# Kernel tuning notes

Hardware: AMD Instinct MI355X
Metric: run time of the kernel (lower is better)

Reference implementation:

```python
import jax, jax.numpy as jnp
import numpy as np

H = 8  # LSTM units, from LSTM_Cell(8)
D = 32  # input feature dim
B = 256
T = 2048


def setup_inputs() -> dict:
    key = jax.random.key(0)
    k1, k2, k3 = jax.random.split(key, 3)
    x = jax.random.normal(k1, (B, T, D), dtype=jnp.float32)
    h0 = jnp.zeros((B, H), dtype=jnp.float32)
    c0 = jnp.zeros((B, H), dtype=jnp.float32)
    # standard LSTM cell params: gate order i, f, g (candidate), o
    Wx = jax.random.normal(k2, (D, 4 * H), dtype=jnp.float32) * (1.0 / np.sqrt(D))
    Wh = jax.random.normal(k3, (H, 4 * H), dtype=jnp.float32) * (1.0 / np.sqrt(H))
    b = jnp.zeros((4 * H,), dtype=jnp.float32)
    return {"x": x, "h0": h0, "c0": c0, "Wx": Wx, "Wh": Wh, "b": b}


def reference(x, h0, c0, Wx, Wh, b):
    """Unrolled LSTM recurrence over time, expressed as a fused lax.scan.

    Returns the per-timestep hidden states [B, T, H] (same math as the
    Python-loop layer, which collects h_t for every t) plus final (h, c).
    """
    xs = jnp.transpose(x, (1, 0, 2))  # [T, B, D]

    def step(carry, xt):
        h, c = carry
        z = xt @ Wx + h @ Wh + b  # [B, 4H]
        i, f, g, o = jnp.split(z, 4, axis=-1)
        i = jax.nn.sigmoid(i)
        f = jax.nn.sigmoid(f)
        g = jnp.tanh(g)
        o = jax.nn.sigmoid(o)
        c_new = f * c + i * g
        h_new = o * jnp.tanh(c_new)
        return (h_new, c_new), h_new

    (h_f, c_f), hs = jax.lax.scan(step, (h0, c0), xs)
    outputs = jnp.transpose(hs, (1, 0, 2))  # [B, T, H]
    return outputs, h_f, c_f
```

## Files before the change

kernel.cpp:

```cpp
#include <hip/hip_runtime.h>
#include <hip/hip_fp16.h>

#define T_STEPS 2048
#define BATCH   256

__device__ __forceinline__ float fexp2(float x) {
#if __has_builtin(__builtin_amdgcn_exp2f)
  return __builtin_amdgcn_exp2f(x);
#else
  return exp2f(x);
#endif
}
__device__ __forceinline__ float frcp(float x) {
#if __has_builtin(__builtin_amdgcn_rcpf)
  return __builtin_amdgcn_rcpf(x);
#else
  return 1.0f / x;
#endif
}

template<int CTRL>
__device__ __forceinline__ float dppf(float x) {
  int i = __float_as_int(x);
  int r = __builtin_amdgcn_update_dpp(i, i, CTRL, 0xF, 0xF, false);
  return __int_as_float(r);
}
#define DPP_X1 0xB1
#define DPP_X2 0x4E
#define DPP_HM 0x141
#define DPP_RM 0x140

#define PIN(x) asm volatile("" : "+v"(x))

#define L2E 1.442695040888963f

__global__ __launch_bounds__(256, 4) void zx_kernel(const float* __restrict__ x,
                                                    const float* __restrict__ Wx,
                                                    const float* __restrict__ bias,
                                                    unsigned* __restrict__ zx) {
  __shared__ float sWx[1024];
  __shared__ float sb[32];
  {
    int t = (int)threadIdx.x;
    for (int i = t; i < 1024; i += 256) sWx[i] = Wx[i];
    if (t < 32) sb[t] = bias[t];
  }
  __syncthreads();

  int wave = (blockIdx.x * 256 + (int)threadIdx.x) >> 6;
  int lane = (int)threadIdx.x & 63;
  int l    = lane & 31;
  int r    = lane >> 5;
  int j    = (l & 3) * 8 + (l >> 2);

  float wxc[32];
#pragma unroll
  for (int d = 0; d < 32; ++d) wxc[d] = sWx[d * 32 + j];
  float bj = sb[j];

  int base = wave * 64;

  for (int it = 0; it < 32; ++it) {
#pragma unroll
    for (int d = 0; d < 32; ++d) PIN(wxc[d]);
    PIN(bj);
    int row = base + (it << 1) + r;
    const float4* xr = (const float4*)(x + (size_t)row * 32);
    float a = bj, b2 = 0.0f;
#pragma unroll
    for (int qq = 0; qq < 8; ++qq) {
      float4 v = xr[qq];
      a  = fmaf(v.x, wxc[4*qq+0], a);
      b2 = fmaf(v.y, wxc[4*qq+1], b2);
      a  = fmaf(v.z, wxc[4*qq+2], a);
      b2 = fmaf(v.w, wxc[4*qq+3], b2);
    }
    float v  = a + b2;
    float pv = dppf<DPP_X1>(v);
    float lo = (l & 1) ? pv : v;
    float hi = (l & 1) ? v  : pv;
    union { _Float16 h2[2]; unsigned u; } pk;
    pk.h2[0] = (_Float16)lo;
    pk.h2[1] = (_Float16)hi;
    zx[(size_t)row * 16 + (l >> 1)] = pk.u;
  }
}

__global__ __launch_bounds__(64, 1) void lstm_kernel(const __half* __restrict__ zx,
                                                     const float* __restrict__ h0,
                                                     const float* __restrict__ c0,
                                                     const float* __restrict__ Wh,
                                                     float* __restrict__ out) {
  __shared__ float sWh[256];
  int lane = (int)threadIdx.x;
  for (int i = lane; i < 256; i += 64) sWh[i] = Wh[i];
  __syncthreads();

  int b = blockIdx.x * 4 + (lane >> 4);
  int q = lane & 15;
  int u = q >> 1;
  int p = q & 1;
  bool pb = (p != 0);

  float wA[8], wB[8];
#pragma unroll
  for (int m = 0; m < 8; ++m) {
    int jrow = u ^ m;
    wA[m] = sWh[jrow * 32 + (2 * p) * 8 + u];
    wB[m] = sWh[jrow * 32 + (2 * p + 1) * 8 + u];
  }
  float cAc = pb ? -2.0f * L2E : -L2E;
  float aAc = pb ? 2.0f : 1.0f;
  float bAc = pb ? -1.0f : 0.0f;

  float h = h0[b * 8 + u];
  float c = c0[b * 8 + u];

  const unsigned* zcur = (const unsigned*)zx + (size_t)b * T_STEPS * 16 + u * 2 + p;
  float*          ocur = out + (size_t)b * T_STEPS * 8 + u;

  constexpr int PD = 8;
  unsigned buf[PD];
#pragma unroll
  for (int pp = 0; pp < PD; ++pp) buf[pp] = zcur[pp * 16];

#define STEP(pp, PRE)                                                        \
  {                                                                          \
    union { unsigned u32; __half2 h2; } zz; zz.u32 = buf[pp];                \
    float2 zf = __half22float2(zz.h2);         \
    if (PRE) buf[pp] = zcur[(pp + PD) * 16];                                 \
    float r0 = h;                                       \
    float r1 = dppf<DPP_X2>(r0);                        \
    float r3 = dppf<DPP_HM>(r0);                        \
    float r7 = dppf<DPP_RM>(r0);                        \
    float r2 = dppf<DPP_X2>(r3);                        \
    float r6 = dppf<DPP_X2>(r7);                        \
    float r4 = dppf<DPP_HM>(r7);                        \
    float r5 = dppf<DPP_X2>(r4);                        \
    float A0 = fmaf(r0, wA[0], zf.x);    \
    float B0 = fmaf(r0, wB[0], zf.y);                                        \
    float A1 = r1 * wA[1];                                                   \
    float B1 = r1 * wB[1];                                                   \
    A1 = fmaf(r3, wA[3], A1);  B1 = fmaf(r3, wB[3], B1);                     \
    A0 = fmaf(r2, wA[2], A0);  B0 = fmaf(r2, wB[2], B0);                     \
    A1 = fmaf(r7, wA[7], A1);  B1 = fmaf(r7, wB[7], B1);                     \
    A0 = fmaf(r6, wA[6], A0);  B0 = fmaf(r6, wB[6], B0);                     \
    A0 = fmaf(r4, wA[4], A0);  B0 = fmaf(r4, wB[4], B0);                     \
    A1 = fmaf(r5, wA[5], A1);  B1 = fmaf(r5, wB[5], B1);                     \
    float A = A0 + A1, B = B0 + B1;                                          \
    float Aact = fmaf(aAc, frcp(1.0f + fexp2(cAc * A)), bAc);                \
    float Bact = frcp(1.0f + fexp2(-L2E * B));                               \
    float A2 = dppf<DPP_X1>(Aact);                                           \
    float B2 = dppf<DPP_X1>(Bact);                                           \
    float iv = pb ? A2   : Aact;                                             \
    float fv = pb ? B2   : Bact;                                             \
    float gv = pb ? Aact : A2;                                               \
    float ov = pb ? Bact : B2;                                               \
    c = fmaf(fv, c, iv * gv);                                                \
    float th = fmaf(2.0f, frcp(1.0f + fexp2(-2.0f * L2E * c)), -1.0f);       \
    h = ov * th;                                                             \
    ocur[pp * 8] = h;            \
  }

  for (int tb = 0; tb < T_STEPS - PD; tb += PD) {
#pragma unroll
    for (int m = 0; m < 8; ++m) { PIN(wA[m]); PIN(wB[m]); }
    PIN(cAc); PIN(aAc); PIN(bAc);
    STEP(0, 1) STEP(1, 1) STEP(2, 1) STEP(3, 1)
    STEP(4, 1) STEP(5, 1) STEP(6, 1) STEP(7, 1)
    zcur += PD * 16;
    ocur += PD * 8;
  }
  STEP(0, 0) STEP(1, 0) STEP(2, 0) STEP(3, 0)
  STEP(4, 0) STEP(5, 0) STEP(6, 0) STEP(7, 0)
#undef STEP

  out[(size_t)BATCH * T_STEPS * 8 +             b * 8 + u] = h;
  out[(size_t)BATCH * T_STEPS * 8 + BATCH * 8 + b * 8 + u] = c;
}

extern "C" void kernel_launch(void* const* d_in, const int* in_sizes, int n_in,
                              void* d_out, int out_size, void* d_ws, size_t ws_size,
                              hipStream_t stream) {
  const float* x    = (const float*)d_in[0];
  const float* h0   = (const float*)d_in[1];
  const float* c0   = (const float*)d_in[2];
  const float* Wx   = (const float*)d_in[3];
  const float* Wh   = (const float*)d_in[4];
  const float* bias = (const float*)d_in[5];
  float* out = (float*)d_out;

  zx_kernel<<<2048, 256, 0, stream>>>(x, Wx, bias, (unsigned*)d_ws);
  lstm_kernel<<<BATCH / 4, 64, 0, stream>>>((const __half*)d_ws, h0, c0, Wh, out);
}
```

Baseline: 421.0 us.

## Hand-schedule LSTM recurrence loop in inline GCN assembly

Replaces the compiler-generated serial LSTM step loop with a hand-written inline-assembly loop. It uses explicit DPP gathers, exp/rcp activations, cndmask gate selection on a precomputed vcc, manual s_nop hazard padding, vmcnt waits and offset-addressed global loads and stores. The aim is to shorten the per-timestep dependency chain and cut scheduling overhead on the latency-bound recurrence. It also rewrites the g gate as 2*sigmoid(2x)-1 fused into the c update and the tanh as fma(2, sig, -o) to save instructions. The risks are fragile hazard handling, hand-placed waitcnts, and 32-bit offsets that must not overflow.

```diff
diff --git a/kernel.cpp b/kernel.cpp
--- a/kernel.cpp
+++ b/kernel.cpp
@@ -3,21 +3,6 @@
 
 #define T_STEPS 2048
 #define BATCH   256
-
-__device__ __forceinline__ float fexp2(float x) {
-#if __has_builtin(__builtin_amdgcn_exp2f)
-  return __builtin_amdgcn_exp2f(x);
-#else
-  return exp2f(x);
-#endif
-}
-__device__ __forceinline__ float frcp(float x) {
-#if __has_builtin(__builtin_amdgcn_rcpf)
-  return __builtin_amdgcn_rcpf(x);
-#else
-  return 1.0f / x;
-#endif
-}
 
 template<int CTRL>
 __device__ __forceinline__ float dppf(float x) {
@@ -26,12 +11,7 @@
   return __int_as_float(r);
 }
 #define DPP_X1 0xB1
-#define DPP_X2 0x4E
-#define DPP_HM 0x141
-#define DPP_RM 0x140
-
 #define PIN(x) asm volatile("" : "+v"(x))
-
 #define L2E 1.442695040888963f
 
 __global__ __launch_bounds__(256, 4) void zx_kernel(const float* __restrict__ x,
@@ -59,7 +39,6 @@
   float bj = sb[j];
 
   int base = wave * 64;
-
   for (int it = 0; it < 32; ++it) {
 #pragma unroll
     for (int d = 0; d < 32; ++d) PIN(wxc[d]);
@@ -86,6 +65,79 @@
   }
 }
 
+
+#define GATHER_DOTS \
+  "v_mov_b32_dpp %[tC], %[h] quad_perm:[2,3,0,1] row_mask:0xf bank_mask:0xf\n\t" \
+  "v_mov_b32_dpp %[tD], %[h] row_half_mirror row_mask:0xf bank_mask:0xf\n\t" \
+  "v_mov_b32_dpp %[tE], %[h] row_mirror row_mask:0xf bank_mask:0xf\n\t" \
+  "v_fmac_f32 %[tA], %[h], %[wA0]\n\t" \
+  "v_fmac_f32 %[tB], %[h], %[wB0]\n\t" \
+  "v_mov_b32_dpp %[tF], %[tD] quad_perm:[2,3,0,1] row_mask:0xf bank_mask:0xf\n\t" \
+  "v_mul_f32 %[tG], %[tC], %[wA1]\n\t" \
+  "v_mul_f32 %[tH], %[tC], %[wB1]\n\t" \
+  "v_mov_b32_dpp %[tC], %[tE] quad_perm:[2,3,0,1] row_mask:0xf bank_mask:0xf\n\t" \
+  "v_fmac_f32 %[tG], %[tD], %[wA3]\n\t" \
+  "v_fmac_f32 %[tH], %[tD], %[wB3]\n\t" \
+  "v_mov_b32_dpp %[tD], %[tE] row_half_mirror row_mask:0xf bank_mask:0xf\n\t" \
+  "v_fmac_f32 %[tA], %[tF], %[wA2]\n\t" \
+  "v_fmac_f32 %[tB], %[tF], %[wB2]\n\t" \
+  "v_fmac_f32 %[tG], %[tE], %[wA7]\n\t" \
+  "v_fmac_f32 %[tH], %[tE], %[wB7]\n\t" \
+  "v_mov_b32_dpp %[tE], %[tD] quad_perm:[2,3,0,1] row_mask:0xf bank_mask:0xf\n\t" \
+  "v_fmac_f32 %[tA], %[tC], %[wA6]\n\t" \
+  "v_fmac_f32 %[tB], %[tC], %[wB6]\n\t" \
+  "v_fmac_f32 %[tA], %[tD], %[wA4]\n\t" \
+  "v_fmac_f32 %[tB], %[tD], %[wB4]\n\t" \
+  "v_fmac_f32 %[tG], %[tE], %[wA5]\n\t" \
+  "v_fmac_f32 %[tH], %[tE], %[wB5]\n\t"
+
+#define ACTPART \
+  "v_add_f32 %[tA], %[tA], %[tG]\n\t" \
+  "v_add_f32 %[tB], %[tB], %[tH]\n\t" \
+  "v_mul_f32 %[tC], %[cAc], %[tA]\n\t" \
+  "v_mul_f32 %[tD], 0xbfb8aa3b, %[tB]\n\t" \
+  "v_exp_f32 %[tC], %[tC]\n\t" \
+  "v_exp_f32 %[tD], %[tD]\n\t" \
+  "s_nop 0\n\t" \
+  "v_add_f32 %[tC], 1.0, %[tC]\n\t" \
+  "v_add_f32 %[tD], 1.0, %[tD]\n\t" \
+  "v_rcp_f32 %[tC], %[tC]\n\t" \
+  "v_rcp_f32 %[tD], %[tD]\n\t" \
+  "s_nop 1\n\t" \
+  "v_mov_b32_dpp %[tE], %[tD] quad_perm:[1,0,3,2] row_mask:0xf bank_mask:0xf\n\t" \
+  "v_mov_b32_dpp %[tF], %[tC] quad_perm:[1,0,3,2] row_mask:0xf bank_mask:0xf\n\t" \
+  "v_cndmask_b32 %[tG], %[tD], %[tE], vcc\n\t" \
+  "v_cndmask_b32 %[tH], %[tE], %[tD], vcc\n\t" \
+  "v_cndmask_b32 %[tE], %[tC], %[tF], vcc\n\t" \
+  "v_mul_f32 %[tF], %[tC], %[tF]\n\t" \
+  "v_fma_f32 %[tF], 2.0, %[tF], -%[tE]\n\t" \
+  "v_fma_f32 %[c], %[tG], %[c], %[tF]\n\t" \
+  "v_mul_f32 %[tA], 0xc038aa3b, %[c]\n\t" \
+  "v_exp_f32 %[tA], %[tA]\n\t" \
+  "s_nop 0\n\t" \
+  "v_add_f32 %[tA], 1.0, %[tA]\n\t" \
+  "v_rcp_f32 %[tA], %[tA]\n\t" \
+  "s_nop 0\n\t" \
+  "v_mul_f32 %[tB], %[tH], %[tA]\n\t" \
+  "v_fma_f32 %[h], 2.0, %[tB], -%[tH]\n\t"
+
+#define LSTEP(K, PF, SO) \
+  "s_waitcnt vmcnt(7)\n\t" \
+  "v_cvt_f32_f16 %[tA], %[b" #K "]\n\t" \
+  "v_lshrrev_b32 %[tB], 16, %[b" #K "]\n\t" \
+  "v_cvt_f32_f16 %[tB], %[tB]\n\t" \
+  "global_load_dword %[b" #K "], %[zoff], %[zb] offset:" #PF "\n\t" \
+  GATHER_DOTS ACTPART \
+  "global_store_dword %[ooff], %[h], %[ob] offset:" #SO "\n\t"
+
+#define ESTEP(K, SO) \
+  "s_waitcnt vmcnt(7)\n\t" \
+  "v_cvt_f32_f16 %[tA], %[b" #K "]\n\t" \
+  "v_lshrrev_b32 %[tB], 16, %[b" #K "]\n\t" \
+  "v_cvt_f32_f16 %[tB], %[tB]\n\t" \
+  GATHER_DOTS ACTPART \
+  "global_store_dword %[ooff], %[h], %[ob] offset:" #SO "\n\t"
+
 __global__ __launch_bounds__(64, 1) void lstm_kernel(const __half* __restrict__ zx,
                                                      const float* __restrict__ h0,
                                                      const float* __restrict__ c0,
@@ -100,7 +152,6 @@
   int q = lane & 15;
   int u = q >> 1;
   int p = q & 1;
-  bool pb = (p != 0);
 
   float wA[8], wB[8];
 #pragma unroll
@@ -109,71 +160,67 @@
     wA[m] = sWh[jrow * 32 + (2 * p) * 8 + u];
     wB[m] = sWh[jrow * 32 + (2 * p + 1) * 8 + u];
   }
-  float cAc = pb ? -2.0f * L2E : -L2E;
-  float aAc = pb ? 2.0f : 1.0f;
-  float bAc = pb ? -1.0f : 0.0f;
+  float cAc = p ? (-2.0f * L2E) : (-L2E);
 
   float h = h0[b * 8 + u];
   float c = c0[b * 8 + u];
 
-  const unsigned* zcur = (const unsigned*)zx + (size_t)b * T_STEPS * 16 + u * 2 + p;
-  float*          ocur = out + (size_t)b * T_STEPS * 8 + u;
-
-  constexpr int PD = 8;
-  unsigned buf[PD];
-#pragma unroll
-  for (int pp = 0; pp < PD; ++pp) buf[pp] = zcur[pp * 16];
-
-#define STEP(pp, PRE)                                                        \
-  {                                                                          \
-    union { unsigned u32; __half2 h2; } zz; zz.u32 = buf[pp];                \
-    float2 zf = __half22float2(zz.h2);         \
-    if (PRE) buf[pp] = zcur[(pp + PD) * 16];                                 \
-    float r0 = h;                                       \
-    float r1 = dppf<DPP_X2>(r0);                        \
-    float r3 = dppf<DPP_HM>(r0);                        \
-    float r7 = dppf<DPP_RM>(r0);                        \
-    float r2 = dppf<DPP_X2>(r3);                        \
-    float r6 = dppf<DPP_X2>(r7);                        \
-    float r4 = dppf<DPP_HM>(r7);                        \
-    float r5 = dppf<DPP_X2>(r4);                        \
-    float A0 = fmaf(r0, wA[0], zf.x);    \
-    float B0 = fmaf(r0, wB[0], zf.y);                                        \
-    float A1 = r1 * wA[1];                                                   \
-    float B1 = r1 * wB[1];                                                   \
-    A1 = fmaf(r3, wA[3], A1);  B1 = fmaf(r3, wB[3], B1);                     \
-    A0 = fmaf(r2, wA[2], A0);  B0 = fmaf(r2, wB[2], B0);                     \
-    A1 = fmaf(r7, wA[7], A1);  B1 = fmaf(r7, wB[7], B1);                     \
-    A0 = fmaf(r6, wA[6], A0);  B0 = fmaf(r6, wB[6], B0);                     \
-    A0 = fmaf(r4, wA[4], A0);  B0 = fmaf(r4, wB[4], B0);                     \
-    A1 = fmaf(r5, wA[5], A1);  B1 = fmaf(r5, wB[5], B1);                     \
-    float A = A0 + A1, B = B0 + B1;                                          \
-    float Aact = fmaf(aAc, frcp(1.0f + fexp2(cAc * A)), bAc);                \
-    float Bact = frcp(1.0f + fexp2(-L2E * B));                               \
-    float A2 = dppf<DPP_X1>(Aact);                                           \
-    float B2 = dppf<DPP_X1>(Bact);                                           \
-    float iv = pb ? A2   : Aact;                                             \
-    float fv = pb ? B2   : Bact;                                             \
-    float gv = pb ? Aact : A2;                                               \
-    float ov = pb ? Bact : B2;                                               \
-    c = fmaf(fv, c, iv * gv);                                                \
-    float th = fmaf(2.0f, frcp(1.0f + fexp2(-2.0f * L2E * c)), -1.0f);       \
-    h = ov * th;                                                             \
-    ocur[pp * 8] = h;            \
-  }
-
-  for (int tb = 0; tb < T_STEPS - PD; tb += PD) {
-#pragma unroll
-    for (int m = 0; m < 8; ++m) { PIN(wA[m]); PIN(wB[m]); }
-    PIN(cAc); PIN(aAc); PIN(bAc);
-    STEP(0, 1) STEP(1, 1) STEP(2, 1) STEP(3, 1)
-    STEP(4, 1) STEP(5, 1) STEP(6, 1) STEP(7, 1)
-    zcur += PD * 16;
-    ocur += PD * 8;
-  }
-  STEP(0, 0) STEP(1, 0) STEP(2, 0) STEP(3, 0)
-  STEP(4, 0) STEP(5, 0) STEP(6, 0) STEP(7, 0)
-#undef STEP
+  const unsigned* zp = (const unsigned*)zx;
+  unsigned zoff = (unsigned)(b * T_STEPS * 64 + u * 8 + p * 4);
+  unsigned ooff = (unsigned)(b * T_STEPS * 32 + u * 4);
+
+  unsigned b0 = zp[(zoff >> 2) + 0 * 16];
+  unsigned b1 = zp[(zoff >> 2) + 1 * 16];
+  unsigned b2 = zp[(zoff >> 2) + 2 * 16];
+  unsigned b3 = zp[(zoff >> 2) + 3 * 16];
+  unsigned b4 = zp[(zoff >> 2) + 4 * 16];
+  unsigned b5 = zp[(zoff >> 2) + 5 * 16];
+  unsigned b6 = zp[(zoff >> 2) + 6 * 16];
+  unsigned b7 = zp[(zoff >> 2) + 7 * 16];
+
+  float tA, tB, tC, tD, tE, tF, tG, tH;
+  int cnt;
+
+  asm volatile(
+    "v_mbcnt_lo_u32_b32 %[tA], -1, 0\n\t"
+    "v_mbcnt_hi_u32_b32 %[tA], -1, %[tA]\n\t"
+    "v_and_b32 %[tA], 1, %[tA]\n\t"
+    "v_cmp_eq_u32 vcc, 1, %[tA]\n\t"
+    "s_mov_b32 %[cnt], 255\n\t"
+    "LSTM_LOOP%=:\n\t"
+    LSTEP(0, 512, 0)
+    LSTEP(1, 576, 32)
+    LSTEP(2, 640, 64)
+    LSTEP(3, 704, 96)
+    LSTEP(4, 768, 128)
+    LSTEP(5, 832, 160)
+    LSTEP(6, 896, 192)
+    LSTEP(7, 960, 224)
+    "v_add_u32 %[zoff], 0x200, %[zoff]\n\t"
+    "v_add_u32 %[ooff], 0x100, %[ooff]\n\t"
+    "s_sub_u32 %[cnt], %[cnt], 1\n\t"
+    "s_cmp_lg_u32 %[cnt], 0\n\t"
+    "s_cbranch_scc1 LSTM_LOOP%=\n\t"
+    ESTEP(0, 0)
+    ESTEP(1, 32)
+    ESTEP(2, 64)
+    ESTEP(3, 96)
+    ESTEP(4, 128)
+    ESTEP(5, 160)
+    ESTEP(6, 192)
+    ESTEP(7, 224)
+    : [h]"+v"(h), [c]"+v"(c), [zoff]"+v"(zoff), [ooff]"+v"(ooff),
+      [b0]"+v"(b0), [b1]"+v"(b1), [b2]"+v"(b2), [b3]"+v"(b3),
+      [b4]"+v"(b4), [b5]"+v"(b5), [b6]"+v"(b6), [b7]"+v"(b7),
+      [tA]"=&v"(tA), [tB]"=&v"(tB), [tC]"=&v"(tC), [tD]"=&v"(tD),
+      [tE]"=&v"(tE), [tF]"=&v"(tF), [tG]"=&v"(tG), [tH]"=&v"(tH),
+      [cnt]"=&s"(cnt)
+    : [wA0]"v"(wA[0]), [wA1]"v"(wA[1]), [wA2]"v"(wA[2]), [wA3]"v"(wA[3]),
+      [wA4]"v"(wA[4]), [wA5]"v"(wA[5]), [wA6]"v"(wA[6]), [wA7]"v"(wA[7]),
+      [wB0]"v"(wB[0]), [wB1]"v"(wB[1]), [wB2]"v"(wB[2]), [wB3]"v"(wB[3]),
+      [wB4]"v"(wB[4]), [wB5]"v"(wB[5]), [wB6]"v"(wB[6]), [wB7]"v"(wB[7]),
+      [cAc]"v"(cAc), [zb]"s"(zp), [ob]"s"(out)
+    : "vcc", "scc", "memory");
 
   out[(size_t)BATCH * T_STEPS * 8 +             b * 8 + u] = h;
   out[(size_t)BATCH * T_STEPS * 8 + BATCH * 8 + b * 8 + u] = c;
```

Result: faster. 401.5 us (-4.6%).
